# Performance work log

Measured on AMD Instinct MI355X. Metric: run time of the kernel, lower is better.

## Reference

```python
import jax, jax.numpy as jnp
import numpy as np

TAU = 0.07  # temperature
B, C, H, W = 8, 128, 512, 512
K = 64      # M sampled queries per image
N_NEG = 7   # num_negatives
P = 4096    # positive prototype pool size


def _l2norm(x, axis=-1, eps=1e-12):
    # matches F.normalize: divide by clamped L2 norm
    n = jnp.sqrt(jnp.sum(x * x, axis=axis, keepdims=True))
    return x / jnp.maximum(n, eps)


def setup_inputs() -> dict:
    key = jax.random.key(0)
    k1, k2, k3, k4 = jax.random.split(key, 4)
    query_feat = jax.random.normal(k1, (B, C, H, W), dtype=jnp.float32)
    pos_pool = jax.random.normal(k2, (P, C), dtype=jnp.float32)
    neg_protos = jax.random.normal(k3, (B, K, N_NEG, C), dtype=jnp.float32)
    query_idx = jax.random.randint(k4, (B, K), 0, H * W)
    return {"query_feat": query_feat, "pos_pool": pos_pool,
            "neg_protos": neg_protos, "query_idx": query_idx}


def reference(query_feat, pos_pool, neg_protos, query_idx):
    b, c, h, w = query_feat.shape
    # gather sampled query pixels: feat.view(C,-1).T -> [B, HW, C] -> [B, K, C]
    feat_flat = query_feat.reshape(b, c, h * w).transpose(0, 2, 1)
    q_pixels = jnp.take_along_axis(feat_flat, query_idx[:, :, None], axis=1)
    q_norm = _l2norm(q_pixels)                      # [B, K, C]

    # positive: top-1 most similar prototype from the pool (cosine sim)
    pool_norm = _l2norm(pos_pool)                   # [P, C]
    sim_pool = jnp.einsum('bkc,pc->bkp', q_norm, pool_norm)
    pos_idx = jnp.argmax(sim_pool, axis=-1)         # [B, K]
    pos_proto = pool_norm[pos_idx]                  # [B, K, C] (already unit-norm)

    neg_norm = _l2norm(neg_protos)                  # [B, K, N, C]

    # protos_all = cat([pos, negs]) along proto dim: [B, K, 1+N, C]
    protos_all = jnp.concatenate([pos_proto[:, :, None, :], neg_norm], axis=2)
    logits_sim = jnp.einsum('bkc,bknc->bkn', q_norm, protos_all) / TAU

    # cross entropy with label 0 (positive first), mean over K per image,
    # then averaged over valid batches (all valid here)
    loss_per = -jax.nn.log_softmax(logits_sim, axis=-1)[..., 0]  # [B, K]
    return jnp.mean(loss_per)
```

## Files before the change

### kernel.cpp

```cpp
#include <hip/hip_runtime.h>
#include <math.h>

#define TAU 0.07f
#define B_ 8
#define C_ 128
#define HW_ (512 * 512)
#define K_ 64
#define NNEG_ 7
#define P_ 4096

__device__ inline float wave_reduce_sum(float v) {
    #pragma unroll
    for (int off = 32; off; off >>= 1) v += __shfl_xor(v, off, 64);
    return v;
}

__device__ inline unsigned long long wave_reduce_maxu64(unsigned long long v) {
    #pragma unroll
    for (int off = 32; off; off >>= 1) {
        unsigned long long o = __shfl_xor(v, off, 64);
        v = (o > v) ? o : v;
    }
    return v;
}

__global__ void normalize_pool_kernel(const float* __restrict__ pool,
                                      float* __restrict__ pool_norm) {
    const int p = blockIdx.x;
    const int c = threadIdx.x;
    __shared__ float red[2];
    float v = pool[p * C_ + c];
    float ws = wave_reduce_sum(v * v);
    const int wid = c >> 6;
    if ((c & 63) == 0) red[wid] = ws;
    __syncthreads();
    const float total = red[0] + red[1];
    const float inv = 1.0f / fmaxf(sqrtf(total), 1e-12f);
    pool_norm[p * C_ + c] = v * inv;
}

__global__ void __launch_bounds__(256)
loss_kernel(const float* __restrict__ qf,
            const float* __restrict__ pool_norm,
            const float* __restrict__ neg,
            const int* __restrict__ qidx,
            float* __restrict__ out) {
    const int bk = blockIdx.x;
    const int b = bk >> 6;
    const int t = threadIdx.x;
    const int wid = t >> 6;

    __shared__ __align__(16) float qn[C_];
    __shared__ float red[8];
    __shared__ unsigned long long redk[4];

    const int idx = qidx[bk];
    float v = 0.0f;
    if (t < C_) v = qf[((size_t)b * C_ + t) * (size_t)HW_ + idx];
    {
        float ws = wave_reduce_sum(v * v);
        if ((t & 63) == 0) red[wid] = ws;
    }
    __syncthreads();
    const float qss = red[0] + red[1] + red[2] + red[3];
    const float qinv = 1.0f / fmaxf(sqrtf(qss), 1e-12f);
    if (t < C_) qn[t] = v * qinv;
    __syncthreads();

    const float4* __restrict__ pn4 = (const float4*)pool_norm;
    const float4* qn4 = (const float4*)qn;
    float best = -3.0e38f;
    int bestp = 0;
    for (int p = t; p < P_; p += 256) {
        const float4* row = pn4 + (size_t)p * (C_ / 4);
        float d = 0.0f;
        #pragma unroll
        for (int i = 0; i < C_ / 4; ++i) {
            float4 a = qn4[i];
            float4 r = row[i];
            d += a.x * r.x + a.y * r.y + a.z * r.z + a.w * r.w;
        }
        if (d > best) { best = d; bestp = p; }
    }
    unsigned int fu = __float_as_uint(best);
    fu = (fu & 0x80000000u) ? ~fu : (fu | 0x80000000u);
    unsigned long long key =
        ((unsigned long long)fu << 32) | (unsigned int)(~(unsigned int)bestp);
    key = wave_reduce_maxu64(key);
    if ((t & 63) == 0) redk[wid] = key;
    __syncthreads();
    if (t == 0) {
        unsigned long long k2 = redk[0];
        #pragma unroll
        for (int i = 1; i < 4; ++i) k2 = (redk[i] > k2) ? redk[i] : k2;
        redk[0] = k2;
    }
    __syncthreads();
    const unsigned long long fkey = redk[0];
    unsigned int vu = (unsigned int)(fkey >> 32);
    vu = (vu & 0x80000000u) ? (vu ^ 0x80000000u) : ~vu;
    const float posdot = __uint_as_float(vu);

    float lg[1 + NNEG_];
    lg[0] = posdot / TAU;
    const float qv = (t < C_) ? qn[t] : 0.0f;
    for (int n = 0; n < NNEG_; ++n) {
        float nv = 0.0f;
        if (t < C_) nv = neg[((size_t)bk * NNEG_ + n) * C_ + t];
        float s1 = wave_reduce_sum(nv * nv);
        float s2 = wave_reduce_sum(nv * qv);
        if ((t & 63) == 0) { red[wid] = s1; red[4 + wid] = s2; }
        __syncthreads();
        if (t == 0) {
            const float nss = red[0] + red[1] + red[2] + red[3];
            const float ndot = red[4] + red[5] + red[6] + red[7];
            lg[1 + n] = (ndot / fmaxf(sqrtf(nss), 1e-12f)) / TAU;
        }
        __syncthreads();
    }

    if (t == 0) {
        float m = lg[0];
        #pragma unroll
        for (int i = 1; i <= NNEG_; ++i) m = fmaxf(m, lg[i]);
        float se = 0.0f;
        #pragma unroll
        for (int i = 0; i <= NNEG_; ++i) se += expf(lg[i] - m);
        const float loss = (m + logf(se)) - lg[0];
        atomicAdd(out, loss * (1.0f / (B_ * K_)));
    }
}

extern "C" void kernel_launch(void* const* d_in, const int* in_sizes, int n_in,
                              void* d_out, int out_size, void* d_ws, size_t ws_size,
                              hipStream_t stream) {
    const float* query_feat = (const float*)d_in[0];
    const float* pos_pool   = (const float*)d_in[1];
    const float* neg_protos = (const float*)d_in[2];
    const int*   query_idx  = (const int*)d_in[3];
    float* out = (float*)d_out;

    float* pool_norm = (float*)d_ws;

    hipMemsetAsync(out, 0, sizeof(float) * out_size, stream);
    normalize_pool_kernel<<<P_, C_, 0, stream>>>(pos_pool, pool_norm);
    loss_kernel<<<B_ * K_, 256, 0, stream>>>(query_feat, pool_norm, neg_protos,
                                             query_idx, out);
}
```

Baseline: 1.268 ms.

## Transpose normalized pool to channel-major for coalesced similarity loads

Result: faster. 1.199 ms (-5.5%).

```diff
diff --git a/kernel.cpp b/kernel.cpp
--- a/kernel.cpp
+++ b/kernel.cpp
@@ -24,24 +24,22 @@
     return v;
 }
 
-__global__ void normalize_pool_kernel(const float* __restrict__ pool,
-                                      float* __restrict__ pool_norm) {
+__global__ void normalize_transpose_kernel(const float* __restrict__ pool,
+                                           float* __restrict__ poolT) {
     const int p = blockIdx.x;
     const int c = threadIdx.x;
     __shared__ float red[2];
     float v = pool[p * C_ + c];
     float ws = wave_reduce_sum(v * v);
-    const int wid = c >> 6;
-    if ((c & 63) == 0) red[wid] = ws;
+    if ((c & 63) == 0) red[c >> 6] = ws;
     __syncthreads();
-    const float total = red[0] + red[1];
-    const float inv = 1.0f / fmaxf(sqrtf(total), 1e-12f);
-    pool_norm[p * C_ + c] = v * inv;
+    const float inv = 1.0f / fmaxf(sqrtf(red[0] + red[1]), 1e-12f);
+    poolT[(size_t)c * P_ + p] = v * inv;
 }
 
 __global__ void __launch_bounds__(256)
 loss_kernel(const float* __restrict__ qf,
-            const float* __restrict__ pool_norm,
+            const float* __restrict__ poolT,
             const float* __restrict__ neg,
             const int* __restrict__ qidx,
             float* __restrict__ out) {
@@ -49,9 +47,11 @@
     const int b = bk >> 6;
     const int t = threadIdx.x;
     const int wid = t >> 6;
+    const int lane = t & 63;
 
     __shared__ __align__(16) float qn[C_];
-    __shared__ float red[8];
+    __shared__ float red[4];
+    __shared__ float lgsh[1 + NNEG_];
     __shared__ unsigned long long redk[4];
 
     const int idx = qidx[bk];
@@ -59,7 +59,7 @@
     if (t < C_) v = qf[((size_t)b * C_ + t) * (size_t)HW_ + idx];
     {
         float ws = wave_reduce_sum(v * v);
-        if ((t & 63) == 0) red[wid] = ws;
+        if (lane == 0) red[wid] = ws;
     }
     __syncthreads();
     const float qss = red[0] + red[1] + red[2] + red[3];
@@ -67,66 +67,66 @@
     if (t < C_) qn[t] = v * qinv;
     __syncthreads();
 
-    const float4* __restrict__ pn4 = (const float4*)pool_norm;
+    const float4* __restrict__ pT4 = (const float4*)poolT;
     const float4* qn4 = (const float4*)qn;
     float best = -3.0e38f;
     int bestp = 0;
-    for (int p = t; p < P_; p += 256) {
-        const float4* row = pn4 + (size_t)p * (C_ / 4);
-        float d = 0.0f;
-        #pragma unroll
-        for (int i = 0; i < C_ / 4; ++i) {
-            float4 a = qn4[i];
-            float4 r = row[i];
-            d += a.x * r.x + a.y * r.y + a.z * r.z + a.w * r.w;
+    #pragma unroll 1
+    for (int j = 0; j < P_ / 1024; ++j) {
+        float4 d; d.x = 0.0f; d.y = 0.0f; d.z = 0.0f; d.w = 0.0f;
+        const float4* __restrict__ col = pT4 + (size_t)j * 256 + t;
+        #pragma unroll 4
+        for (int cc = 0; cc < C_ / 4; ++cc) {
+            const float4 qv = qn4[cc];
+            const float4 v0 = col[(size_t)(4 * cc + 0) * (P_ / 4)];
+            const float4 v1 = col[(size_t)(4 * cc + 1) * (P_ / 4)];
+            const float4 v2 = col[(size_t)(4 * cc + 2) * (P_ / 4)];
+            const float4 v3 = col[(size_t)(4 * cc + 3) * (P_ / 4)];
+            d.x += qv.x * v0.x + qv.y * v1.x + qv.z * v2.x + qv.w * v3.x;
+            d.y += qv.x * v0.y + qv.y * v1.y + qv.z * v2.y + qv.w * v3.y;
+            d.z += qv.x * v0.z + qv.y * v1.z + qv.z * v2.z + qv.w * v3.z;
+            d.w += qv.x * v0.w + qv.y * v1.w + qv.z * v2.w + qv.w * v3.w;
         }
-        if (d > best) { best = d; bestp = p; }
+        const int pb = (j * 256 + t) * 4;
+        if (d.x > best) { best = d.x; bestp = pb + 0; }
+        if (d.y > best) { best = d.y; bestp = pb + 1; }
+        if (d.z > best) { best = d.z; bestp = pb + 2; }
+        if (d.w > best) { best = d.w; bestp = pb + 3; }
     }
     unsigned int fu = __float_as_uint(best);
     fu = (fu & 0x80000000u) ? ~fu : (fu | 0x80000000u);
     unsigned long long key =
         ((unsigned long long)fu << 32) | (unsigned int)(~(unsigned int)bestp);
     key = wave_reduce_maxu64(key);
-    if ((t & 63) == 0) redk[wid] = key;
+    if (lane == 0) redk[wid] = key;
+
+    const float2* __restrict__ qn2 = (const float2*)qn;
+    const float2 q2 = qn2[lane];
+    const float2* __restrict__ neg2 =
+        (const float2*)(neg + (size_t)bk * NNEG_ * C_);
+    for (int n = wid; n < NNEG_; n += 4) {
+        const float2 nv = neg2[n * (C_ / 2) + lane];
+        float s1 = wave_reduce_sum(nv.x * nv.x + nv.y * nv.y);
+        float s2 = wave_reduce_sum(nv.x * q2.x + nv.y * q2.y);
+        if (lane == 0)
+            lgsh[1 + n] = (s2 / fmaxf(sqrtf(s1), 1e-12f)) * (1.0f / TAU);
+    }
     __syncthreads();
+
     if (t == 0) {
         unsigned long long k2 = redk[0];
         #pragma unroll
         for (int i = 1; i < 4; ++i) k2 = (redk[i] > k2) ? redk[i] : k2;
-        redk[0] = k2;
-    }
-    __syncthreads();
-    const unsigned long long fkey = redk[0];
-    unsigned int vu = (unsigned int)(fkey >> 32);
-    vu = (vu & 0x80000000u) ? (vu ^ 0x80000000u) : ~vu;
-    const float posdot = __uint_as_float(vu);
-
-    float lg[1 + NNEG_];
-    lg[0] = posdot / TAU;
-    const float qv = (t < C_) ? qn[t] : 0.0f;
-    for (int n = 0; n < NNEG_; ++n) {
-        float nv = 0.0f;
-        if (t < C_) nv = neg[((size_t)bk * NNEG_ + n) * C_ + t];
-        float s1 = wave_reduce_sum(nv * nv);
-        float s2 = wave_reduce_sum(nv * qv);
-        if ((t & 63) == 0) { red[wid] = s1; red[4 + wid] = s2; }
-        __syncthreads();
-        if (t == 0) {
-            const float nss = red[0] + red[1] + red[2] + red[3];
-            const float ndot = red[4] + red[5] + red[6] + red[7];
-            lg[1 + n] = (ndot / fmaxf(sqrtf(nss), 1e-12f)) / TAU;
-        }
-        __syncthreads();
-    }
-
-    if (t == 0) {
-        float m = lg[0];
+        unsigned int vu = (unsigned int)(k2 >> 32);
+        vu = (vu & 0x80000000u) ? (vu ^ 0x80000000u) : ~vu;
+        float lg0 = __uint_as_float(vu) * (1.0f / TAU);
+        float m = lg0;
         #pragma unroll
-        for (int i = 1; i <= NNEG_; ++i) m = fmaxf(m, lg[i]);
-        float se = 0.0f;
+        for (int i = 1; i <= NNEG_; ++i) m = fmaxf(m, lgsh[i]);
+        float se = expf(lg0 - m);
         #pragma unroll
-        for (int i = 0; i <= NNEG_; ++i) se += expf(lg[i] - m);
-        const float loss = (m + logf(se)) - lg[0];
+        for (int i = 1; i <= NNEG_; ++i) se += expf(lgsh[i] - m);
+        const float loss = (m + logf(se)) - lg0;
         atomicAdd(out, loss * (1.0f / (B_ * K_)));
     }
 }
@@ -140,10 +140,10 @@
     const int*   query_idx  = (const int*)d_in[3];
     float* out = (float*)d_out;
 
-    float* pool_norm = (float*)d_ws;
+    float* poolT = (float*)d_ws;
 
     hipMemsetAsync(out, 0, sizeof(float) * out_size, stream);
-    normalize_pool_kernel<<<P_, C_, 0, stream>>>(pos_pool, pool_norm);
-    loss_kernel<<<B_ * K_, 256, 0, stream>>>(query_feat, pool_norm, neg_protos,
+    normalize_transpose_kernel<<<P_, C_, 0, stream>>>(pos_pool, poolT);
+    loss_kernel<<<B_ * K_, 256, 0, stream>>>(query_feat, poolT, neg_protos,
                                              query_idx, out);
 }
```
